# Performance work log

Hardware: AMD Instinct MI355X
Metric: run time of the kernel (lower is better)

## Reference

```python
import jax, jax.numpy as jnp
import numpy as np

DEPTH_VALID_MIN = 1e-4   # cfg.depth_valid_min
IOU_THRESH = 0.02        # cfg.collision_iou_thresh
TOPK = 64                # cfg.collision_topk


def setup_inputs() -> dict:
    key = jax.random.key(0)
    k1, k2, k3, k4 = jax.random.split(key, 4)
    N, H, W = 128, 512, 512
    boxes = jax.random.uniform(k1, (N, 4), dtype=jnp.float32)
    masks = jax.random.uniform(k2, (N, H, W), dtype=jnp.float32)
    conf = jax.random.uniform(k3, (N,), dtype=jnp.float32)
    depth = jax.random.uniform(k4, (H, W), dtype=jnp.float32)
    return {"boxes": boxes, "masks": masks, "conf": conf, "depth": depth}


def _mask_depth_var(depth, mask):
    # population variance of depth pixels where mask>0.5 and depth>valid_min
    valid = (mask > 0.5) & (depth > DEPTH_VALID_MIN)
    cnt = jnp.sum(valid)
    cntf = jnp.maximum(cnt, 1).astype(depth.dtype)
    mean = jnp.sum(jnp.where(valid, depth, 0.0)) / cntf
    var = jnp.sum(jnp.where(valid, (depth - mean) ** 2, 0.0)) / cntf
    return jnp.where(cnt > 0, var, 0.0)


def reference(boxes, masks, conf, depth):
    N = boxes.shape[0]
    x1, y1, x2, y2 = boxes[:, 0], boxes[:, 1], boxes[:, 2], boxes[:, 3]
    bw = jnp.maximum(x2 - x1, 0.0)
    bh = jnp.maximum(y2 - y1, 0.0)
    area = jnp.clip(bw * bh, 0.0, 1.0)

    # per-detection masked depth variance (vectorized over N)
    d_var = jax.vmap(lambda m: _mask_depth_var(depth, m))(masks)  # [N]

    tall = jnp.clip(bh / (bw + 1e-6), 0.0, 10.0)
    thinness = jax.nn.sigmoid((tall - 1.2) * 2.0)
    unstable = jnp.clip(0.35 * thinness + 0.35 * jax.nn.sigmoid(d_var * 6.0)
                        + 0.3 * (1.0 - conf), 0.0, 1.0)
    slip = jnp.clip(0.45 * jax.nn.sigmoid(d_var * 8.0) + 0.25 * (1.0 - conf)
                    + 0.3 * jax.nn.sigmoid((area - 0.05) * 3.0), 0.0, 1.0)
    support = jnp.clip(1.0 - unstable, 0.0, 1.0)

    # pairwise IoU [N,N]
    xx1 = jnp.maximum(x1[:, None], x1[None, :])
    yy1 = jnp.maximum(y1[:, None], y1[None, :])
    xx2 = jnp.minimum(x2[:, None], x2[None, :])
    yy2 = jnp.minimum(y2[:, None], y2[None, :])
    inter = jnp.maximum(xx2 - xx1, 0.0) * jnp.maximum(yy2 - yy1, 0.0)
    a = bw * bh
    union = a[:, None] + a[None, :] - inter
    iou = inter / (union + 1e-6)
    iou = iou * (1.0 - jnp.eye(N, dtype=iou.dtype))  # fill_diagonal_(0)

    # collision pairs: top-k over off-diagonal IoUs above threshold (padded to TOPK)
    flat = iou.ravel()
    masked = jnp.where(flat > IOU_THRESH, flat, -1.0)
    vals, idx = jax.lax.top_k(masked, TOPK)
    valid = vals > IOU_THRESH
    pairs = jnp.where(valid[:, None],
                      jnp.stack([idx // N, idx % N], axis=-1), 0).astype(jnp.int32)
    collision = jnp.where(valid, jnp.clip(vals * 5.0, 0.0, 1.0), 0.0)

    return unstable, slip, support, pairs, collision
```

## Files before the change

### kernel.cpp

```cpp
#include <hip/hip_runtime.h>
#include <stdint.h>

#define N_BOX 128
#define HW    262144
#define SPLIT 16
#define CHUNK (HW / SPLIT)
#define TOPK  64
typedef unsigned long long u64;

__global__ __launch_bounds__(256) void k_mask_partial(
    const float* __restrict__ masks, const float* __restrict__ depth,
    float* __restrict__ part) {
  const int b = blockIdx.x;
  const int m = b >> 4;
  const int s = b & (SPLIT - 1);
  const float4* mk = reinterpret_cast<const float4*>(masks + (size_t)m * HW + (size_t)s * CHUNK);
  const float4* dp = reinterpret_cast<const float4*>(depth + (size_t)s * CHUNK);
  const int t = threadIdx.x;

  float c = 0.f, s1 = 0.f, s2 = 0.f;
#pragma unroll
  for (int j = 0; j < 16; ++j) {
    const int i = t + j * 256;
    float4 mv = mk[i];
    float4 dv = dp[i];
    if (mv.x > 0.5f && dv.x > 1e-4f) { c += 1.f; s1 += dv.x; s2 += dv.x * dv.x; }
    if (mv.y > 0.5f && dv.y > 1e-4f) { c += 1.f; s1 += dv.y; s2 += dv.y * dv.y; }
    if (mv.z > 0.5f && dv.z > 1e-4f) { c += 1.f; s1 += dv.z; s2 += dv.z * dv.z; }
    if (mv.w > 0.5f && dv.w > 1e-4f) { c += 1.f; s1 += dv.w; s2 += dv.w * dv.w; }
  }
  for (int off = 32; off > 0; off >>= 1) {
    c  += __shfl_down(c,  off);
    s1 += __shfl_down(s1, off);
    s2 += __shfl_down(s2, off);
  }
  __shared__ float red[3][4];
  const int wid = t >> 6, lane = t & 63;
  if (lane == 0) { red[0][wid] = c; red[1][wid] = s1; red[2][wid] = s2; }
  __syncthreads();
  if (t == 0) {
    part[b * 3 + 0] = red[0][0] + red[0][1] + red[0][2] + red[0][3];
    part[b * 3 + 1] = red[1][0] + red[1][1] + red[1][2] + red[1][3];
    part[b * 3 + 2] = red[2][0] + red[2][1] + red[2][2] + red[2][3];
  }
}

__device__ __forceinline__ u64 sort64_desc(u64 v, int lane) {
#pragma unroll
  for (int size = 2; size <= 64; size <<= 1) {
#pragma unroll
    for (int stride = size >> 1; stride > 0; stride >>= 1) {
      const u64 o = __shfl_xor(v, stride);
      const bool blk   = ((lane & size) == 0);
      const bool lower = ((lane & stride) == 0);
      const u64 mx = (v > o) ? v : o;
      const u64 mn = (v > o) ? o : v;
      v = (blk == lower) ? mx : mn;
    }
  }
  return v;
}

__device__ __forceinline__ u64 merge64_desc(u64 v, u64 s, int lane) {
  const u64 r = __shfl_xor(s, 63);
  v = (v > r) ? v : r;
#pragma unroll
  for (int stride = 32; stride > 0; stride >>= 1) {
    const u64 o = __shfl_xor(v, stride);
    const bool lower = ((lane & stride) == 0);
    const u64 mx = (v > o) ? v : o;
    const u64 mn = (v > o) ? o : v;
    v = lower ? mx : mn;
  }
  return v;
}

__device__ __forceinline__ float sigf(float x) { return 1.f / (1.f + expf(-x)); }

__global__ __launch_bounds__(1024) void k_topk_fin(
    const float* __restrict__ boxes, const float* __restrict__ conf,
    const float* __restrict__ part, float* __restrict__ out) {
  __shared__ float X1[N_BOX], Y1[N_BOX], X2[N_BOX], Y2[N_BOX], A[N_BOX];
  __shared__ u64 wtop[16][TOPK];
  __shared__ u64 wcand[16][TOPK];

  const int t = threadIdx.x;
  const int lane = t & 63;
  const int w = t >> 6;

  if (t < N_BOX) {
    const float x1 = boxes[t * 4 + 0], y1 = boxes[t * 4 + 1];
    const float x2 = boxes[t * 4 + 2], y2 = boxes[t * 4 + 3];
    X1[t] = x1; Y1[t] = y1; X2[t] = x2; Y2[t] = y2;
    A[t] = fmaxf(x2 - x1, 0.f) * fmaxf(y2 - y1, 0.f);
  }
  __syncthreads();

  u64 run = 0ULL;
  int nbuf = 0;
#pragma unroll
  for (int b = 0; b < 16; ++b) {
    const int e = w * 1024 + b * 64 + lane;
    const int i = e >> 7, jj = e & 127;
    const float xx1 = fmaxf(X1[i], X1[jj]);
    const float yy1 = fmaxf(Y1[i], Y1[jj]);
    const float xx2 = fminf(X2[i], X2[jj]);
    const float yy2 = fminf(Y2[i], Y2[jj]);
    const float inter = fmaxf(xx2 - xx1, 0.f) * fmaxf(yy2 - yy1, 0.f);
    const float uni = A[i] + A[jj] - inter;
    float iou = inter / (uni + 1e-6f);
    if (i == jj) iou = 0.f;
    const bool cand = (iou > 0.02f);
    const float mval = cand ? iou : -1.0f;
    uint32_t u = __float_as_uint(mval);
    u = (u & 0x80000000u) ? ~u : (u | 0x80000000u);
    const u64 key = ((u64)u << 32) | (u64)(0xFFFFFFFFu - (uint32_t)e);

    if (b == 0) {
      run = sort64_desc(key, lane);
    } else {
      const u64 mask = __ballot(cand);
      const int nc = __popcll(mask);
      if ((w == 0 && b == 1) || (nbuf + nc > TOPK)) {
        run = merge64_desc(run, sort64_desc(key, lane), lane);
      } else if (nc) {
        const int pos = nbuf + __popcll(mask & ((1ULL << lane) - 1ULL));
        if (cand) wcand[w][pos] = key;
        nbuf += nc;
      }
    }
  }
  if (nbuf > 0) {
    const u64 k = (lane < nbuf) ? wcand[w][lane] : 0ULL;
    run = merge64_desc(run, sort64_desc(k, lane), lane);
  }
  wtop[w][lane] = run;
  __syncthreads();

  for (int n = 8; n >= 1; n >>= 1) {
    u64 a = 0ULL, bb = 0ULL;
    if (w < n) { a = wtop[2 * w][lane]; bb = wtop[2 * w + 1][lane]; }
    __syncthreads();
    if (w < n) wtop[w][lane] = merge64_desc(a, bb, lane);
    __syncthreads();
  }

  if (w == 0) {
    const u64 v = wtop[0][lane];
    const uint32_t mh = (uint32_t)(v >> 32);
    const uint32_t u  = (mh & 0x80000000u) ? (mh ^ 0x80000000u) : ~mh;
    const float val   = __uint_as_float(u);
    const uint32_t e  = 0xFFFFFFFFu - (uint32_t)(v & 0xFFFFFFFFu);
    const bool valid  = (val > 0.02f);
    out[3 * N_BOX + 2 * lane + 0] = valid ? (float)(e >> 7)  : 0.f;
    out[3 * N_BOX + 2 * lane + 1] = valid ? (float)(e & 127) : 0.f;
    out[3 * N_BOX + 2 * TOPK + lane] = valid ? fminf(fmaxf(val * 5.f, 0.f), 1.f) : 0.f;
  } else if (w == 2 || w == 3) {
    const int m = t - 128;
    float C = 0.f, S1 = 0.f, S2 = 0.f;
#pragma unroll
    for (int s = 0; s < SPLIT; ++s) {
      C  += part[(m * SPLIT + s) * 3 + 0];
      S1 += part[(m * SPLIT + s) * 3 + 1];
      S2 += part[(m * SPLIT + s) * 3 + 2];
    }
    const float cntf = fmaxf(C, 1.f);
    const float mean = S1 / cntf;
    float var = S2 / cntf - mean * mean;
    var = (C > 0.f) ? fmaxf(var, 0.f) : 0.f;

    const float x1 = X1[m], y1 = Y1[m], x2 = X2[m], y2 = Y2[m];
    const float bw = fmaxf(x2 - x1, 0.f);
    const float bh = fmaxf(y2 - y1, 0.f);
    const float area = fminf(fmaxf(bw * bh, 0.f), 1.f);
    const float cf = conf[m];
    const float tall = fminf(fmaxf(bh / (bw + 1e-6f), 0.f), 10.f);
    const float thin = sigf((tall - 1.2f) * 2.f);
    const float unst = fminf(fmaxf(0.35f * thin + 0.35f * sigf(var * 6.f) + 0.3f * (1.f - cf), 0.f), 1.f);
    const float slip = fminf(fmaxf(0.45f * sigf(var * 8.f) + 0.25f * (1.f - cf) + 0.3f * sigf((area - 0.05f) * 3.f), 0.f), 1.f);
    out[m]             = unst;
    out[N_BOX + m]     = slip;
    out[2 * N_BOX + m] = fminf(fmaxf(1.f - unst, 0.f), 1.f);
  }
}

extern "C" void kernel_launch(void* const* d_in, const int* in_sizes, int n_in,
                              void* d_out, int out_size, void* d_ws, size_t ws_size,
                              hipStream_t stream) {
  const float* boxes = (const float*)d_in[0];
  const float* masks = (const float*)d_in[1];
  const float* conf  = (const float*)d_in[2];
  const float* depth = (const float*)d_in[3];
  float* out  = (float*)d_out;
  float* part = (float*)d_ws;

  hipLaunchKernelGGL(k_mask_partial, dim3(N_BOX * SPLIT), dim3(256), 0, stream,
                     masks, depth, part);
  hipLaunchKernelGGL(k_topk_fin, dim3(1), dim3(1024), 0, stream,
                     boxes, conf, part, out);
}
```

Before: 209.5 us.

## Run top-k in block 0 of the mask-reduction kernel, split finalize out

The pairwise-IoU top-k selection now runs in block 0 of the large mask-reduction launch, so it overlaps with the bandwidth-bound masked depth reduction instead of running serially afterward. The per-box finalize (variance, sigmoids, outputs) moves into a small separate 128-thread kernel. Mask blocks grow from 256 to 1024 threads, each doing 4 float4 loads per thread instead of 16. This raises per-block parallelism but reduces loads in flight per thread, and the large block size with the sort's shared memory may limit occupancy.

```diff
diff --git a/kernel.cpp b/kernel.cpp
--- a/kernel.cpp
+++ b/kernel.cpp
@@ -6,44 +6,8 @@
 #define SPLIT 16
 #define CHUNK (HW / SPLIT)
 #define TOPK  64
+#define NMASKBLK (N_BOX * SPLIT)
 typedef unsigned long long u64;
-
-__global__ __launch_bounds__(256) void k_mask_partial(
-    const float* __restrict__ masks, const float* __restrict__ depth,
-    float* __restrict__ part) {
-  const int b = blockIdx.x;
-  const int m = b >> 4;
-  const int s = b & (SPLIT - 1);
-  const float4* mk = reinterpret_cast<const float4*>(masks + (size_t)m * HW + (size_t)s * CHUNK);
-  const float4* dp = reinterpret_cast<const float4*>(depth + (size_t)s * CHUNK);
-  const int t = threadIdx.x;
-
-  float c = 0.f, s1 = 0.f, s2 = 0.f;
-#pragma unroll
-  for (int j = 0; j < 16; ++j) {
-    const int i = t + j * 256;
-    float4 mv = mk[i];
-    float4 dv = dp[i];
-    if (mv.x > 0.5f && dv.x > 1e-4f) { c += 1.f; s1 += dv.x; s2 += dv.x * dv.x; }
-    if (mv.y > 0.5f && dv.y > 1e-4f) { c += 1.f; s1 += dv.y; s2 += dv.y * dv.y; }
-    if (mv.z > 0.5f && dv.z > 1e-4f) { c += 1.f; s1 += dv.z; s2 += dv.z * dv.z; }
-    if (mv.w > 0.5f && dv.w > 1e-4f) { c += 1.f; s1 += dv.w; s2 += dv.w * dv.w; }
-  }
-  for (int off = 32; off > 0; off >>= 1) {
-    c  += __shfl_down(c,  off);
-    s1 += __shfl_down(s1, off);
-    s2 += __shfl_down(s2, off);
-  }
-  __shared__ float red[3][4];
-  const int wid = t >> 6, lane = t & 63;
-  if (lane == 0) { red[0][wid] = c; red[1][wid] = s1; red[2][wid] = s2; }
-  __syncthreads();
-  if (t == 0) {
-    part[b * 3 + 0] = red[0][0] + red[0][1] + red[0][2] + red[0][3];
-    part[b * 3 + 1] = red[1][0] + red[1][1] + red[1][2] + red[1][3];
-    part[b * 3 + 2] = red[2][0] + red[2][1] + red[2][2] + red[2][3];
-  }
-}
 
 __device__ __forceinline__ u64 sort64_desc(u64 v, int lane) {
 #pragma unroll
@@ -77,9 +41,11 @@
 
 __device__ __forceinline__ float sigf(float x) { return 1.f / (1.f + expf(-x)); }
 
-__global__ __launch_bounds__(1024) void k_topk_fin(
-    const float* __restrict__ boxes, const float* __restrict__ conf,
-    const float* __restrict__ part, float* __restrict__ out) {
+__global__ __launch_bounds__(1024) void k_fused(
+    const float* __restrict__ boxes, const float* __restrict__ masks,
+    const float* __restrict__ depth, float* __restrict__ part,
+    float* __restrict__ out) {
+  __shared__ float red[3][16];
   __shared__ float X1[N_BOX], Y1[N_BOX], X2[N_BOX], Y2[N_BOX], A[N_BOX];
   __shared__ u64 wtop[16][TOPK];
   __shared__ u64 wcand[16][TOPK];
@@ -87,6 +53,42 @@
   const int t = threadIdx.x;
   const int lane = t & 63;
   const int w = t >> 6;
+
+  if (blockIdx.x != 0) {
+    const int b = blockIdx.x - 1;
+    const int m = b >> 4;
+    const int s = b & (SPLIT - 1);
+    const float4* mk = reinterpret_cast<const float4*>(masks + (size_t)m * HW + (size_t)s * CHUNK);
+    const float4* dp = reinterpret_cast<const float4*>(depth + (size_t)s * CHUNK);
+
+    float c = 0.f, s1 = 0.f, s2 = 0.f;
+#pragma unroll
+    for (int j = 0; j < 4; ++j) {
+      const int i = t + j * 1024;
+      const float4 mv = mk[i];
+      const float4 dv = dp[i];
+      if (mv.x > 0.5f && dv.x > 1e-4f) { c += 1.f; s1 += dv.x; s2 += dv.x * dv.x; }
+      if (mv.y > 0.5f && dv.y > 1e-4f) { c += 1.f; s1 += dv.y; s2 += dv.y * dv.y; }
+      if (mv.z > 0.5f && dv.z > 1e-4f) { c += 1.f; s1 += dv.z; s2 += dv.z * dv.z; }
+      if (mv.w > 0.5f && dv.w > 1e-4f) { c += 1.f; s1 += dv.w; s2 += dv.w * dv.w; }
+    }
+    for (int off = 32; off > 0; off >>= 1) {
+      c  += __shfl_down(c,  off);
+      s1 += __shfl_down(s1, off);
+      s2 += __shfl_down(s2, off);
+    }
+    if (lane == 0) { red[0][w] = c; red[1][w] = s1; red[2][w] = s2; }
+    __syncthreads();
+    if (t == 0) {
+      float C = 0.f, S1 = 0.f, S2 = 0.f;
+#pragma unroll
+      for (int k = 0; k < 16; ++k) { C += red[0][k]; S1 += red[1][k]; S2 += red[2][k]; }
+      part[b * 3 + 0] = C;
+      part[b * 3 + 1] = S1;
+      part[b * 3 + 2] = S2;
+    }
+    return;
+  }
 
   if (t < N_BOX) {
     const float x1 = boxes[t * 4 + 0], y1 = boxes[t * 4 + 1];
@@ -155,33 +157,38 @@
     out[3 * N_BOX + 2 * lane + 0] = valid ? (float)(e >> 7)  : 0.f;
     out[3 * N_BOX + 2 * lane + 1] = valid ? (float)(e & 127) : 0.f;
     out[3 * N_BOX + 2 * TOPK + lane] = valid ? fminf(fmaxf(val * 5.f, 0.f), 1.f) : 0.f;
-  } else if (w == 2 || w == 3) {
-    const int m = t - 128;
-    float C = 0.f, S1 = 0.f, S2 = 0.f;
-#pragma unroll
-    for (int s = 0; s < SPLIT; ++s) {
-      C  += part[(m * SPLIT + s) * 3 + 0];
-      S1 += part[(m * SPLIT + s) * 3 + 1];
-      S2 += part[(m * SPLIT + s) * 3 + 2];
-    }
-    const float cntf = fmaxf(C, 1.f);
-    const float mean = S1 / cntf;
-    float var = S2 / cntf - mean * mean;
-    var = (C > 0.f) ? fmaxf(var, 0.f) : 0.f;
-
-    const float x1 = X1[m], y1 = Y1[m], x2 = X2[m], y2 = Y2[m];
-    const float bw = fmaxf(x2 - x1, 0.f);
-    const float bh = fmaxf(y2 - y1, 0.f);
-    const float area = fminf(fmaxf(bw * bh, 0.f), 1.f);
-    const float cf = conf[m];
-    const float tall = fminf(fmaxf(bh / (bw + 1e-6f), 0.f), 10.f);
-    const float thin = sigf((tall - 1.2f) * 2.f);
-    const float unst = fminf(fmaxf(0.35f * thin + 0.35f * sigf(var * 6.f) + 0.3f * (1.f - cf), 0.f), 1.f);
-    const float slip = fminf(fmaxf(0.45f * sigf(var * 8.f) + 0.25f * (1.f - cf) + 0.3f * sigf((area - 0.05f) * 3.f), 0.f), 1.f);
-    out[m]             = unst;
-    out[N_BOX + m]     = slip;
-    out[2 * N_BOX + m] = fminf(fmaxf(1.f - unst, 0.f), 1.f);
-  }
+  }
+}
+
+__global__ __launch_bounds__(128) void k_finalize(
+    const float* __restrict__ boxes, const float* __restrict__ conf,
+    const float* __restrict__ part, float* __restrict__ out) {
+  const int m = threadIdx.x;
+  float C = 0.f, S1 = 0.f, S2 = 0.f;
+#pragma unroll
+  for (int s = 0; s < SPLIT; ++s) {
+    C  += part[(m * SPLIT + s) * 3 + 0];
+    S1 += part[(m * SPLIT + s) * 3 + 1];
+    S2 += part[(m * SPLIT + s) * 3 + 2];
+  }
+  const float cntf = fmaxf(C, 1.f);
+  const float mean = S1 / cntf;
+  float var = S2 / cntf - mean * mean;
+  var = (C > 0.f) ? fmaxf(var, 0.f) : 0.f;
+
+  const float x1 = boxes[m * 4 + 0], y1 = boxes[m * 4 + 1];
+  const float x2 = boxes[m * 4 + 2], y2 = boxes[m * 4 + 3];
+  const float bw = fmaxf(x2 - x1, 0.f);
+  const float bh = fmaxf(y2 - y1, 0.f);
+  const float area = fminf(fmaxf(bw * bh, 0.f), 1.f);
+  const float cf = conf[m];
+  const float tall = fminf(fmaxf(bh / (bw + 1e-6f), 0.f), 10.f);
+  const float thin = sigf((tall - 1.2f) * 2.f);
+  const float unst = fminf(fmaxf(0.35f * thin + 0.35f * sigf(var * 6.f) + 0.3f * (1.f - cf), 0.f), 1.f);
+  const float slip = fminf(fmaxf(0.45f * sigf(var * 8.f) + 0.25f * (1.f - cf) + 0.3f * sigf((area - 0.05f) * 3.f), 0.f), 1.f);
+  out[m]             = unst;
+  out[N_BOX + m]     = slip;
+  out[2 * N_BOX + m] = fminf(fmaxf(1.f - unst, 0.f), 1.f);
 }
 
 extern "C" void kernel_launch(void* const* d_in, const int* in_sizes, int n_in,
@@ -194,8 +201,8 @@
   float* out  = (float*)d_out;
   float* part = (float*)d_ws;
 
-  hipLaunchKernelGGL(k_mask_partial, dim3(N_BOX * SPLIT), dim3(256), 0, stream,
-                     masks, depth, part);
-  hipLaunchKernelGGL(k_topk_fin, dim3(1), dim3(1024), 0, stream,
+  hipLaunchKernelGGL(k_fused, dim3(NMASKBLK + 1), dim3(1024), 0, stream,
+                     boxes, masks, depth, part, out);
+  hipLaunchKernelGGL(k_finalize, dim3(1), dim3(128), 0, stream,
                      boxes, conf, part, out);
 }
```

Measured after the change: 195.5 us. -6.7%, faster.
